# Performance work log

Measured on AMD Instinct MI355X. Metric: run time of the kernel, lower is better.

Reference implementation:

```python
import jax, jax.numpy as jnp
import numpy as np

B, L, D = 16, 256, 256        # batch, enc positions, enc_out_dim
H, E, V, T = 256, 256, 172, 128  # dec_rnn_h, emb_size, vocab, target_len
INIT = 0.01


def setup_inputs() -> dict:
    key = jax.random.key(0)
    ks = jax.random.split(key, 20)
    u = lambda k, shape, s: jax.random.uniform(k, shape, jnp.float32, -s, s)
    inp = {
        "imgs": jax.random.normal(ks[0], (B, L, D), jnp.float32),
        "target_list": jax.random.randint(ks[1], (B, T), 0, V),
        # embedding + LSTMCell (torch layout: W_ih [4H, H+E], W_hh [4H, H])
        "emb": jax.random.normal(ks[2], (V, E), jnp.float32) * 0.02,
        "W_ih": u(ks[3], (4 * H, H + E), 1.0 / np.sqrt(H)),
        "W_hh": u(ks[4], (4 * H, H), 1.0 / np.sqrt(H)),
        "b_ih": u(ks[5], (4 * H,), 1.0 / np.sqrt(H)),
        "b_hh": u(ks[6], (4 * H,), 1.0 / np.sqrt(H)),
        # attention / output projections (no bias)
        "W1": u(ks[7], (D, D), 1.0 / np.sqrt(D)),
        "W2": u(ks[8], (D, H), 1.0 / np.sqrt(H)),
        "W3": u(ks[9], (H, H + D), 1.0 / np.sqrt(H + D)),
        "Wout": u(ks[10], (V, H), 1.0 / np.sqrt(H)),
        "beta": u(ks[11], (D,), INIT),
        # init decoder linears (with bias)
        "wh_W": u(ks[12], (H, D), 1.0 / np.sqrt(D)),
        "wh_b": u(ks[13], (H,), 1.0 / np.sqrt(D)),
        "wc_W": u(ks[14], (H, D), 1.0 / np.sqrt(D)),
        "wc_b": u(ks[15], (H,), 1.0 / np.sqrt(D)),
        "wo_W": u(ks[16], (H, D), 1.0 / np.sqrt(D)),
        "wo_b": u(ks[17], (H,), 1.0 / np.sqrt(D)),
    }
    return inp


def _forward(imgs, emb, W_ih, W_hh, b_ih, b_hh, W1, W2, W3, Wout, beta,
             wh_W, wh_b, wc_W, wc_b, wo_W, wo_b, target_list):
    # init states from mean-pooled encoder output
    mean_enc = imgs.mean(axis=1)                       # [B, D]
    h = jnp.tanh(mean_enc @ wh_W.T + wh_b)             # [B, H]
    c = jnp.tanh(mean_enc @ wc_W.T + wc_b)
    o = jnp.tanh(mean_enc @ wo_W.T + wo_b)

    enc_proj = jnp.einsum('bld,ed->ble', imgs, W1)     # W_1(enc_out), step-invariant

    def step(carry, tgt_t):
        h, c, o = carry
        prev_y = emb[tgt_t]                            # [B, E]
        inp = jnp.concatenate([prev_y, o], axis=1)     # [B, E+H]
        gates = inp @ W_ih.T + b_ih + h @ W_hh.T + b_hh  # [B, 4H]
        i_g, f_g, g_g, o_g = jnp.split(gates, 4, axis=1)
        c_new = jax.nn.sigmoid(f_g) * c + jax.nn.sigmoid(i_g) * jnp.tanh(g_g)
        h_new = jax.nn.sigmoid(o_g) * jnp.tanh(c_new)
        # Bahdanau attention
        alpha = jnp.tanh(enc_proj + (h_new @ W2.T)[:, None, :])   # [B, L, D]
        score = jnp.einsum('bld,d->bl', alpha, beta)
        attn = jax.nn.softmax(score, axis=-1)                     # [B, L]
        ctx = jnp.einsum('bl,bld->bd', attn, imgs)                # [B, D]
        o_new = jnp.tanh(jnp.concatenate([h_new, ctx], axis=1) @ W3.T)  # [B, H]
        logit = jax.nn.softmax(o_new @ Wout.T, axis=1)            # [B, V]
        return (h_new, c_new, o_new), logit

    _, logits = jax.lax.scan(step, (h, c, o), target_list.T)      # [T, B, V]
    return jnp.transpose(logits, (1, 0, 2))                       # [B, T, V]


def reference(imgs, target_list, emb, W_ih, W_hh, b_ih, b_hh, W1, W2, W3,
              Wout, beta, wh_W, wh_b, wc_W, wc_b, wo_W, wo_b):
    return _forward(imgs, emb, W_ih, W_hh, b_ih, b_hh, W1, W2, W3, Wout, beta,
                    wh_W, wh_b, wc_W, wc_b, wo_W, wo_b, target_list)
```

## Files before the change

### kernel.cpp

```cpp
#include <hip/hip_runtime.h>

typedef unsigned int u32;


#define OFF_BAR   0ull
#define OFF_PSE   16384ull
#define OFF_STH   65536ull
#define OFF_PQH   98304ull
#define OFF_PCTX  622592ull
#define OFF_OALL  1146880ull
#define OFF_GTOK  3244032ull

__device__ __forceinline__ float sigm(float x){ return 1.0f/(1.0f+__expf(-x)); }
__device__ __forceinline__ float tanh_f(float x){ return 1.0f - 2.0f/(1.0f+__expf(2.0f*x)); }

__device__ __forceinline__ float blo(u32 q){ u32 x = q<<16; float f; __builtin_memcpy(&f,&x,4); return f; }
__device__ __forceinline__ float bhi(u32 q){ u32 x = q & 0xffff0000u; float f; __builtin_memcpy(&f,&x,4); return f; }
__device__ __forceinline__ u32 f2bu(float f){ u32 x; __builtin_memcpy(&x,&f,4); x = x + 0x7fffu + ((x>>16)&1u); return x>>16; }

struct F8 { float v[8]; };
__device__ __forceinline__ F8 ld8f(const float* q){
  F8 r; float4 a = *(const float4*)q; float4 b = *(const float4*)(q+4);
  r.v[0]=a.x;r.v[1]=a.y;r.v[2]=a.z;r.v[3]=a.w;r.v[4]=b.x;r.v[5]=b.y;r.v[6]=b.z;r.v[7]=b.w;
  return r;
}
__device__ __forceinline__ float dot8(const F8& w, const float* x){
  float4 a = *(const float4*)x; float4 b = *(const float4*)(x+4);
  return w.v[0]*a.x + w.v[1]*a.y + w.v[2]*a.z + w.v[3]*a.w
       + w.v[4]*b.x + w.v[5]*b.y + w.v[6]*b.z + w.v[7]*b.w;
}
__device__ __forceinline__ float dot8r(const float* wr, const float* x){
  float4 a = *(const float4*)x; float4 b = *(const float4*)(x+4);
  return wr[0]*a.x + wr[1]*a.y + wr[2]*a.z + wr[3]*a.w
       + wr[4]*b.x + wr[5]*b.y + wr[6]*b.z + wr[7]*b.w;
}

__device__ __forceinline__ float cohload(const float* p){
  u32 x = __hip_atomic_load((const u32*)p, __ATOMIC_RELAXED, __HIP_MEMORY_SCOPE_AGENT);
  float f; __builtin_memcpy(&f,&x,4); return f;
}
__device__ __forceinline__ void cohstore(float* p, float v){
  u32 x; __builtin_memcpy(&x,&v,4);
  __hip_atomic_store((u32*)p, x, __ATOMIC_RELAXED, __HIP_MEMORY_SCOPE_AGENT);
}

__device__ __forceinline__ void wait_flags(u32* gf, u32 seq){
  if (threadIdx.x < 16){
    while (__hip_atomic_load(gf + threadIdx.x*16, __ATOMIC_RELAXED, __HIP_MEMORY_SCOPE_AGENT) < seq){
      __builtin_amdgcn_s_sleep(1);
    }
  }
  __syncthreads();
}
__device__ __forceinline__ void publish_flag(u32* myf, u32 seq){
  __hip_atomic_store(myf, seq, __ATOMIC_RELEASE, __HIP_MEMORY_SCOPE_AGENT);
}
__device__ __forceinline__ void publish_flag_fast(u32* myf, u32 seq){
  asm volatile("s_waitcnt vmcnt(0)" ::: "memory");
  __hip_atomic_store(myf, seq, __ATOMIC_RELAXED, __HIP_MEMORY_SCOPE_AGENT);
}

extern "C" __global__ __launch_bounds__(256)
void k_init(char* __restrict__ ws){
  u32* bar = (u32*)(ws + OFF_BAR);
  const int gt = blockIdx.x*256 + threadIdx.x;
  if (gt < 4096) bar[gt] = 0u;
}

extern "C" __global__ __launch_bounds__(256, 1)
void k_main(const float* __restrict__ imgs, const int* __restrict__ tgt,
            const float* __restrict__ emb,  const float* __restrict__ W_ih,
            const float* __restrict__ W_hh, const float* __restrict__ b_ih,
            const float* __restrict__ b_hh, const float* __restrict__ W1,
            const float* __restrict__ W2,   const float* __restrict__ W3,
            const float* __restrict__ beta, const float* __restrict__ whW,
            const float* __restrict__ whb,  const float* __restrict__ wcW,
            const float* __restrict__ wcb,  const float* __restrict__ woW,
            const float* __restrict__ wob,  char* __restrict__ ws)
{
  const int tid = threadIdx.x, bid = blockIdx.x;
  const int g = bid & 15, w = bid >> 4, u0 = w*16;

  u32* gf   = (u32*)(ws + OFF_BAR) + g*256;
  u32* myf  = gf + w*16;
  float* stH  = (float*)(ws + OFF_STH);
  float* pQH  = (float*)(ws + OFF_PQH);
  float* pCTX = (float*)(ws + OFF_PCTX);
  float* pSE  = (float*)(ws + OFF_PSE);
  float* oAll = (float*)(ws + OFF_OALL);
  float* gtok = (float*)(ws + OFF_GTOK);

  __shared__ __align__(16) float sImg[16*256];
  __shared__ __align__(16) float sEnc[16*256];
  __shared__ __align__(16) float sPimg[16*256];
  __shared__ __align__(16) float sPool[768];
  __shared__ __align__(16) float sHprev[256];
  __shared__ __align__(16) float sO[256];
  __shared__ __align__(16) float sHw2[256];
  __shared__ float sBeta[256];
  __shared__ float sG[64];
  __shared__ float sHown[16];
  __shared__ float sC[16];
  __shared__ float sE[16];
  __shared__ float sE2[16];

  sBeta[tid] = beta[tid];

  for (int r=0; r<3; r++){
    const int tk = bid + 256*r;
    __syncthreads();
    if (tk < 688){
      const int v = tk>>2, q = tk&3;
      sPool[512 + tid] = emb[(size_t)v*256 + tid];
      __syncthreads();
      const int j = q*256 + tid;
      const float* wr = W_ih + (size_t)j*512;
      float a = 0.f;
      #pragma unroll 8
      for (int c=0; c<32; c++) a += dot8(ld8f(wr + c*8), sPool + 512 + c*8);
      gtok[(size_t)v*1024 + j] = a + b_ih[j] + b_hh[j];
    } else {
      __syncthreads();
    }
  }
  __syncthreads();

  { const size_t r0 = (size_t)(g*256 + w*16);
    for (int ri=0; ri<16; ri++) sImg[ri*256+tid] = imgs[(r0+ri)*256 + tid];
    __syncthreads();
    { float acc[16];
      #pragma unroll
      for (int ri=0; ri<16; ri++) acc[ri]=0.f;
      const float* w1r = W1 + (size_t)tid*256;
      for (int c=0; c<32; c++){
        F8 wv = ld8f(w1r + c*8);
        #pragma unroll
        for (int ri=0; ri<16; ri++) acc[ri] += dot8(wv, sImg + ri*256 + c*8);
      }
      for (int ri=0; ri<16; ri++) sEnc[ri*256+tid] = acc[ri];
    }
    { float acc[16];
      #pragma unroll
      for (int ri=0; ri<16; ri++) acc[ri]=0.f;
      const float* w3cr = W3 + (size_t)tid*512 + 256;
      for (int c=0; c<32; c++){
        F8 wv = ld8f(w3cr + c*8);
        #pragma unroll
        for (int ri=0; ri<16; ri++) acc[ri] += dot8(wv, sImg + ri*256 + c*8);
      }
      for (int ri=0; ri<16; ri++) sPimg[ri*256+tid] = acc[ri];
    }
  }
  __syncthreads();

  { float m = 0.f;
    for (int l=0; l<256; l++) m += imgs[((size_t)g*256 + l)*256 + tid];
    sPool[tid] = m * (1.0f/256.0f);
  }
  __syncthreads();
  { const float* whr = whW + (size_t)tid*256;
    const float* wor = woW + (size_t)tid*256;
    float ah=0.f, ao=0.f;
    for (int c=0; c<32; c++){
      ah += dot8(ld8f(whr + c*8), sPool + c*8);
      ao += dot8(ld8f(wor + c*8), sPool + c*8);
    }
    sHprev[tid] = tanhf(ah + whb[tid]);
    sO[tid]     = tanhf(ao + wob[tid]);
  }
  { const int j = tid>>4, sub = tid&15, u = u0 + j;
    float ac=0.f;
    #pragma unroll
    for (int c=0; c<2; c++)
      ac += dot8(ld8f(wcW + (size_t)u*256 + sub*16 + c*8), sPool + sub*16 + c*8);
    ac += __shfl_xor(ac,1); ac += __shfl_xor(ac,2); ac += __shfl_xor(ac,4); ac += __shfl_xor(ac,8);
    if (sub == 0) sC[j] = tanhf(ac + wcb[u]);
  }

  const int rl = tid>>2, p = tid&3;
  const int unit = rl & 15, gate = rl >> 4;
  const int grow = gate*256 + u0 + unit;
  float wior[64], whhr[64];
  { const float* wio = W_ih + (size_t)grow*512 + 256 + p*64;
    const float* whh = W_hh + (size_t)grow*256 +       p*64;
    #pragma unroll
    for (int c=0; c<8; c++){
      F8 a = ld8f(wio + c*8);
      F8 b = ld8f(whh + c*8);
      #pragma unroll
      for (int i=0; i<8; i++){ wior[c*8+i] = a.v[i]; whhr[c*8+i] = b.v[i]; }
    }
  }
  u32 w2p[128];
  { const float* w2r = W2 + (size_t)tid*256;
    #pragma unroll
    for (int c=0; c<128; c++)
      w2p[c] = f2bu(w2r[2*c]) | (f2bu(w2r[2*c+1]) << 16);
  }
  float w3h[16];
  { F8 a = ld8f(W3 + (size_t)tid*512 + u0);
    F8 b = ld8f(W3 + (size_t)tid*512 + u0 + 8);
    #pragma unroll
    for (int i=0; i<8; i++){ w3h[i] = a.v[i]; w3h[8+i] = b.v[i]; }
  }
  const int* tgt_g = tgt + g*128;
  const float* gtok_row = gtok + grow;

  __syncthreads();
  if (tid == 0) publish_flag(myf, 1u);
  wait_flags(gf, 1u);

  float hpart = 0.f;
  { const float* xh = sHprev + p*64;
    #pragma unroll
    for (int c=0; c<8; c++) hpart += dot8r(whhr + c*8, xh + c*8);
  }

  for (int t=0; t<128; t++){
    const int par = t & 1;
    const int y = tgt_g[t];
    const float gyv = gtok_row[(size_t)y*1024];

    { float acc = hpart;
      const float* xo = sO + p*64;
      #pragma unroll
      for (int c=0; c<8; c++) acc += dot8r(wior + c*8, xo + c*8);
      acc += __shfl_xor(acc, 1); acc += __shfl_xor(acc, 2);
      if (p == 0) sG[rl] = acc + gyv;
    }
    __syncthreads();
    if (tid < 16){
      float ig = sG[tid], fg = sG[16+tid], gg = sG[32+tid], og = sG[48+tid];
      float cn = sigm(fg)*sC[tid] + sigm(ig)*tanh_f(gg);
      float hn = sigm(og)*tanh_f(cn);
      sC[tid] = cn;
      sHown[tid] = hn;
      cohstore(stH + par*4096 + g*256 + u0 + tid, hn);
      if (tid == 0) publish_flag_fast(myf, 2u*t + 2u);
    }
    __syncthreads();
    { float qh = 0.f;
      #pragma unroll
      for (int k=0; k<16; k++) qh += w3h[k] * sHown[k];
      cohstore(pQH + ((size_t)(par*16 + g)*16 + w)*256 + tid, qh);
    }

    wait_flags(gf, 2u*t + 2u);
    sHprev[tid] = cohload(stH + par*4096 + g*256 + tid);
    __syncthreads();
    { float a = 0.f;
      #pragma unroll
      for (int c=0; c<128; c++){
        u32 q = w2p[c];
        a += blo(q)*sHprev[2*c] + bhi(q)*sHprev[2*c+1];
      }
      sHw2[tid] = a;
    }
    __syncthreads();
    { const int li = tid>>4, sub = tid&15;
      const float* ep = sEnc + li*256;
      float sc = 0.f;
      #pragma unroll
      for (int i=0; i<16; i++){ int d = i*16 + sub; sc += tanh_f(ep[d] + sHw2[d]) * sBeta[d]; }
      sc += __shfl_xor(sc,1); sc += __shfl_xor(sc,2); sc += __shfl_xor(sc,4); sc += __shfl_xor(sc,8);
      if (sub == 0) sE[li] = __expf(sc);
    }
    __syncthreads();
    { float pv = 0.f;
      #pragma unroll
      for (int li2=0; li2<16; li2++) pv += sE[li2] * sPimg[li2*256 + tid];
      cohstore(pCTX + ((size_t)g*16 + w)*256 + tid, pv);
    }
    if (tid == 0){
      float se = 0.f;
      #pragma unroll
      for (int j=0; j<16; j++) se += sE[j];
      cohstore(pSE + g*16 + w, se);
    }
    __syncthreads();
    if (tid == 0) publish_flag_fast(myf, 2u*t + 3u);

    wait_flags(gf, 2u*t + 3u);
    if (tid < 16) sE2[tid] = cohload(pSE + g*16 + tid);
    float qh = 0.f, pvs = 0.f;
    { const float* qb = pQH  + (size_t)(par*16 + g)*4096 + tid;
      const float* cb = pCTX + (size_t)g*4096 + tid;
      #pragma unroll
      for (int j=0; j<16; j++){ qh += cohload(qb + j*256); pvs += cohload(cb + j*256); }
    }
    __syncthreads();
    { float se = 0.f;
      #pragma unroll
      for (int j=0; j<16; j++) se += sE2[j];
      float o = tanh_f(qh + pvs/se);
      sO[tid] = o;
      if ((tid>>4) == w) oAll[((size_t)t*16 + g)*256 + tid] = o;
    }
    { float hp2 = 0.f;
      const float* xh = sHprev + p*64;
      #pragma unroll
      for (int c=0; c<8; c++) hp2 += dot8r(whhr + c*8, xh + c*8);
      hpart = hp2;
    }
    __syncthreads();
  }
}

extern "C" __global__ __launch_bounds__(256)
void k_logits(const float* __restrict__ Wout, char* __restrict__ ws, float* __restrict__ out){
  __shared__ __align__(16) float sO_[256];
  __shared__ __align__(16) float sRed[256];
  const int tid = threadIdx.x, q = blockIdx.x;
  const int b = q >> 7, t = q & 127;
  const float* oAll = (const float*)(ws + OFF_OALL);
  sO_[tid] = oAll[((size_t)t*16 + b)*256 + tid];
  __syncthreads();
  float lg = 0.f;
  if (tid < 172){
    const float* wr = Wout + (size_t)tid*256;
    #pragma unroll 8
    for (int c=0; c<32; c++) lg += dot8(ld8f(wr + c*8), sO_ + c*8);
  }
  sRed[tid] = (tid < 172) ? lg : -1e30f;
  __syncthreads();
  for (int s2=128; s2>0; s2>>=1){ if (tid < s2) sRed[tid] = fmaxf(sRed[tid], sRed[tid+s2]); __syncthreads(); }
  const float mx = sRed[0];
  __syncthreads();
  const float ev = (tid < 172) ? __expf(lg - mx) : 0.f;
  sRed[tid] = ev;
  __syncthreads();
  for (int s2=128; s2>0; s2>>=1){ if (tid < s2) sRed[tid] += sRed[tid+s2]; __syncthreads(); }
  const float inv = 1.0f / sRed[0];
  if (tid < 172) out[((size_t)b*128 + t)*172 + tid] = ev * inv;
}

extern "C" void kernel_launch(void* const* d_in, const int* in_sizes, int n_in,
                              void* d_out, int out_size, void* d_ws, size_t ws_size,
                              hipStream_t stream) {
  (void)in_sizes; (void)n_in; (void)out_size; (void)ws_size;
  char* ws = (char*)d_ws;
  k_init<<<16, 256, 0, stream>>>(ws);
  k_main<<<256, 256, 0, stream>>>(
      (const float*)d_in[0],  (const int*)d_in[1],  (const float*)d_in[2],
      (const float*)d_in[3],  (const float*)d_in[4], (const float*)d_in[5],
      (const float*)d_in[6],  (const float*)d_in[7], (const float*)d_in[8],
      (const float*)d_in[9],  (const float*)d_in[11], (const float*)d_in[12],
      (const float*)d_in[13], (const float*)d_in[14], (const float*)d_in[15],
      (const float*)d_in[16], (const float*)d_in[17], ws);
  k_logits<<<2048, 256, 0, stream>>>((const float*)d_in[10], ws, (float*)d_out);
}
```

Baseline: 1.462 ms.

## Repartition recurrent kernel into 8 wider blocks per batch with 512 threads

Changes the persistent recurrent kernel from 256 blocks of 256 threads (16 blocks per batch row, 16 hidden units each) to 128 blocks of 512 threads (8 blocks per batch row, 32 units each). Cross-block flag waits and partial-sum reductions (qh, ctx, softmax denominators) shrink from 16 to 8 contributors, which cuts inter-block synchronisation and coherent global traffic per timestep. Thread pairs now split dot products and combine them with shuffles, and the W_hh partial for the next step is moved ahead of the second publish. The cost is larger shared memory per block and more register pressure at 512 threads, which could lower occupancy or force spills.

```diff
diff --git a/kernel.cpp b/kernel.cpp
--- a/kernel.cpp
+++ b/kernel.cpp
@@ -5,11 +5,11 @@
 
 #define OFF_BAR   0ull
 #define OFF_PSE   16384ull
-#define OFF_STH   65536ull
-#define OFF_PQH   98304ull
-#define OFF_PCTX  622592ull
-#define OFF_OALL  1146880ull
-#define OFF_GTOK  3244032ull
+#define OFF_STH   32768ull
+#define OFF_PQH   65536ull
+#define OFF_PCTX  327680ull
+#define OFF_OALL  458752ull
+#define OFF_GTOK  2555904ull
 
 __device__ __forceinline__ float sigm(float x){ return 1.0f/(1.0f+__expf(-x)); }
 __device__ __forceinline__ float tanh_f(float x){ return 1.0f - 2.0f/(1.0f+__expf(2.0f*x)); }
@@ -45,7 +45,7 @@
 }
 
 __device__ __forceinline__ void wait_flags(u32* gf, u32 seq){
-  if (threadIdx.x < 16){
+  if (threadIdx.x < 8){
     while (__hip_atomic_load(gf + threadIdx.x*16, __ATOMIC_RELAXED, __HIP_MEMORY_SCOPE_AGENT) < seq){
       __builtin_amdgcn_s_sleep(1);
     }
@@ -64,10 +64,10 @@
 void k_init(char* __restrict__ ws){
   u32* bar = (u32*)(ws + OFF_BAR);
   const int gt = blockIdx.x*256 + threadIdx.x;
-  if (gt < 4096) bar[gt] = 0u;
-}
-
-extern "C" __global__ __launch_bounds__(256, 1)
+  if (gt < 2048) bar[gt] = 0u;
+}
+
+extern "C" __global__ __launch_bounds__(512, 2)
 void k_main(const float* __restrict__ imgs, const int* __restrict__ tgt,
             const float* __restrict__ emb,  const float* __restrict__ W_ih,
             const float* __restrict__ W_hh, const float* __restrict__ b_ih,
@@ -79,9 +79,9 @@
             const float* __restrict__ wob,  char* __restrict__ ws)
 {
   const int tid = threadIdx.x, bid = blockIdx.x;
-  const int g = bid & 15, w = bid >> 4, u0 = w*16;
-
-  u32* gf   = (u32*)(ws + OFF_BAR) + g*256;
+  const int g = bid & 15, w = bid >> 4, u0 = w*32;
+
+  u32* gf   = (u32*)(ws + OFF_BAR) + g*128;
   u32* myf  = gf + w*16;
   float* stH  = (float*)(ws + OFF_STH);
   float* pQH  = (float*)(ws + OFF_PQH);
@@ -90,34 +90,34 @@
   float* oAll = (float*)(ws + OFF_OALL);
   float* gtok = (float*)(ws + OFF_GTOK);
 
-  __shared__ __align__(16) float sImg[16*256];
-  __shared__ __align__(16) float sEnc[16*256];
-  __shared__ __align__(16) float sPimg[16*256];
-  __shared__ __align__(16) float sPool[768];
+  __shared__ __align__(16) float sImg[32*256];
+  __shared__ __align__(16) float sEnc[32*256];
+  __shared__ __align__(16) float sPimg[32*256];
+  __shared__ __align__(16) float sPool[256];
   __shared__ __align__(16) float sHprev[256];
   __shared__ __align__(16) float sO[256];
   __shared__ __align__(16) float sHw2[256];
   __shared__ float sBeta[256];
-  __shared__ float sG[64];
-  __shared__ float sHown[16];
-  __shared__ float sC[16];
-  __shared__ float sE[16];
-  __shared__ float sE2[16];
-
-  sBeta[tid] = beta[tid];
+  __shared__ float sG[128];
+  __shared__ float sHown[32];
+  __shared__ float sC[32];
+  __shared__ float sE[32];
+  __shared__ float sE2[8];
+
+  if (tid < 256) sBeta[tid] = beta[tid];
 
   for (int r=0; r<3; r++){
-    const int tk = bid + 256*r;
-    __syncthreads();
-    if (tk < 688){
-      const int v = tk>>2, q = tk&3;
-      sPool[512 + tid] = emb[(size_t)v*256 + tid];
+    const int tk = bid + 128*r;
+    __syncthreads();
+    if (tk < 344){
+      const int v = tk>>1, h2 = tk&1;
+      if (tid < 256) sPool[tid] = emb[(size_t)v*256 + tid];
       __syncthreads();
-      const int j = q*256 + tid;
+      const int j = h2*512 + tid;
       const float* wr = W_ih + (size_t)j*512;
       float a = 0.f;
       #pragma unroll 8
-      for (int c=0; c<32; c++) a += dot8(ld8f(wr + c*8), sPool + 512 + c*8);
+      for (int c=0; c<32; c++) a += dot8(ld8f(wr + c*8), sPool + c*8);
       gtok[(size_t)v*1024 + j] = a + b_ih[j] + b_hh[j];
     } else {
       __syncthreads();
@@ -125,61 +125,70 @@
   }
   __syncthreads();
 
-  { const size_t r0 = (size_t)(g*256 + w*16);
-    for (int ri=0; ri<16; ri++) sImg[ri*256+tid] = imgs[(r0+ri)*256 + tid];
+  { const size_t r0 = (size_t)(g*256 + w*32);
+    const int dcol = tid & 255, rh = tid >> 8;
+    for (int ri=0; ri<16; ri++)
+      sImg[(rh*16+ri)*256 + dcol] = imgs[(r0 + rh*16 + ri)*256 + dcol];
     __syncthreads();
     { float acc[16];
       #pragma unroll
       for (int ri=0; ri<16; ri++) acc[ri]=0.f;
-      const float* w1r = W1 + (size_t)tid*256;
+      const float* w1r = W1 + (size_t)dcol*256;
       for (int c=0; c<32; c++){
         F8 wv = ld8f(w1r + c*8);
         #pragma unroll
-        for (int ri=0; ri<16; ri++) acc[ri] += dot8(wv, sImg + ri*256 + c*8);
-      }
-      for (int ri=0; ri<16; ri++) sEnc[ri*256+tid] = acc[ri];
+        for (int ri=0; ri<16; ri++) acc[ri] += dot8(wv, sImg + (rh*16+ri)*256 + c*8);
+      }
+      for (int ri=0; ri<16; ri++) sEnc[(rh*16+ri)*256 + dcol] = acc[ri];
     }
     { float acc[16];
       #pragma unroll
       for (int ri=0; ri<16; ri++) acc[ri]=0.f;
-      const float* w3cr = W3 + (size_t)tid*512 + 256;
+      const float* w3cr = W3 + (size_t)dcol*512 + 256;
       for (int c=0; c<32; c++){
         F8 wv = ld8f(w3cr + c*8);
         #pragma unroll
-        for (int ri=0; ri<16; ri++) acc[ri] += dot8(wv, sImg + ri*256 + c*8);
-      }
-      for (int ri=0; ri<16; ri++) sPimg[ri*256+tid] = acc[ri];
-    }
-  }
-  __syncthreads();
-
-  { float m = 0.f;
-    for (int l=0; l<256; l++) m += imgs[((size_t)g*256 + l)*256 + tid];
-    sPool[tid] = m * (1.0f/256.0f);
-  }
-  __syncthreads();
-  { const float* whr = whW + (size_t)tid*256;
-    const float* wor = woW + (size_t)tid*256;
+        for (int ri=0; ri<16; ri++) acc[ri] += dot8(wv, sImg + (rh*16+ri)*256 + c*8);
+      }
+      for (int ri=0; ri<16; ri++) sPimg[(rh*16+ri)*256 + dcol] = acc[ri];
+    }
+  }
+  __syncthreads();
+
+  { const int d = tid>>1, lh = tid&1;
+    float m = 0.f;
+    for (int l=lh*128; l<lh*128+128; l++) m += imgs[((size_t)g*256 + l)*256 + d];
+    m += __shfl_xor(m, 1);
+    if (lh == 0) sPool[d] = m * (1.0f/256.0f);
+  }
+  __syncthreads();
+  { const int u = tid>>1, ch = tid&1;
+    const float* whr = whW + (size_t)u*256 + ch*128;
+    const float* wor = woW + (size_t)u*256 + ch*128;
     float ah=0.f, ao=0.f;
-    for (int c=0; c<32; c++){
-      ah += dot8(ld8f(whr + c*8), sPool + c*8);
-      ao += dot8(ld8f(wor + c*8), sPool + c*8);
-    }
-    sHprev[tid] = tanhf(ah + whb[tid]);
-    sO[tid]     = tanhf(ao + wob[tid]);
-  }
-  { const int j = tid>>4, sub = tid&15, u = u0 + j;
+    for (int c=0; c<16; c++){
+      ah += dot8(ld8f(whr + c*8), sPool + ch*128 + c*8);
+      ao += dot8(ld8f(wor + c*8), sPool + ch*128 + c*8);
+    }
+    ah += __shfl_xor(ah,1); ao += __shfl_xor(ao,1);
+    if (ch == 0){
+      sHprev[u] = tanhf(ah + whb[u]);
+      sO[u]     = tanhf(ao + wob[u]);
+    }
+  }
+  { const int ul = tid>>4, sub = tid&15;
+    const int u = u0 + ul;
     float ac=0.f;
     #pragma unroll
     for (int c=0; c<2; c++)
       ac += dot8(ld8f(wcW + (size_t)u*256 + sub*16 + c*8), sPool + sub*16 + c*8);
     ac += __shfl_xor(ac,1); ac += __shfl_xor(ac,2); ac += __shfl_xor(ac,4); ac += __shfl_xor(ac,8);
-    if (sub == 0) sC[j] = tanhf(ac + wcb[u]);
+    if (sub == 0) sC[ul] = tanhf(ac + wcb[u]);
   }
 
   const int rl = tid>>2, p = tid&3;
-  const int unit = rl & 15, gate = rl >> 4;
-  const int grow = gate*256 + u0 + unit;
+  const int ul_g = rl & 31, gate = rl >> 5;
+  const int grow = gate*256 + u0 + ul_g;
   float wior[64], whhr[64];
   { const float* wio = W_ih + (size_t)grow*512 + 256 + p*64;
     const float* whh = W_hh + (size_t)grow*256 +       p*64;
@@ -191,15 +200,17 @@
       for (int i=0; i<8; i++){ wior[c*8+i] = a.v[i]; whhr[c*8+i] = b.v[i]; }
     }
   }
-  u32 w2p[128];
-  { const float* w2r = W2 + (size_t)tid*256;
-    #pragma unroll
-    for (int c=0; c<128; c++)
+  const int d2 = tid>>1, ch2 = tid&1;
+  u32 w2p[64];
+  { const float* w2r = W2 + (size_t)d2*256 + ch2*128;
+    #pragma unroll
+    for (int c=0; c<64; c++)
       w2p[c] = f2bu(w2r[2*c]) | (f2bu(w2r[2*c+1]) << 16);
   }
+  const int uq = tid>>1, kh = tid&1;
   float w3h[16];
-  { F8 a = ld8f(W3 + (size_t)tid*512 + u0);
-    F8 b = ld8f(W3 + (size_t)tid*512 + u0 + 8);
+  { F8 a = ld8f(W3 + (size_t)uq*512 + u0 + kh*16);
+    F8 b = ld8f(W3 + (size_t)uq*512 + u0 + kh*16 + 8);
     #pragma unroll
     for (int i=0; i<8; i++){ w3h[i] = a.v[i]; w3h[8+i] = b.v[i]; }
   }
@@ -229,8 +240,8 @@
       if (p == 0) sG[rl] = acc + gyv;
     }
     __syncthreads();
-    if (tid < 16){
-      float ig = sG[tid], fg = sG[16+tid], gg = sG[32+tid], og = sG[48+tid];
+    if (tid < 32){
+      float ig = sG[tid], fg = sG[32+tid], gg = sG[64+tid], og = sG[96+tid];
       float cn = sigm(fg)*sC[tid] + sigm(ig)*tanh_f(gg);
       float hn = sigm(og)*tanh_f(cn);
       sC[tid] = cn;
@@ -241,20 +252,23 @@
     __syncthreads();
     { float qh = 0.f;
       #pragma unroll
-      for (int k=0; k<16; k++) qh += w3h[k] * sHown[k];
-      cohstore(pQH + ((size_t)(par*16 + g)*16 + w)*256 + tid, qh);
+      for (int i=0; i<16; i++) qh += w3h[i] * sHown[kh*16 + i];
+      qh += __shfl_xor(qh, 1);
+      if (kh == 0) cohstore(pQH + ((size_t)(par*16 + g)*8 + w)*256 + uq, qh);
     }
 
     wait_flags(gf, 2u*t + 2u);
-    sHprev[tid] = cohload(stH + par*4096 + g*256 + tid);
+    if (tid < 256) sHprev[tid] = cohload(stH + par*4096 + g*256 + tid);
     __syncthreads();
     { float a = 0.f;
-      #pragma unroll
-      for (int c=0; c<128; c++){
+      const float* hb = sHprev + ch2*128;
+      #pragma unroll
+      for (int c=0; c<64; c++){
         u32 q = w2p[c];
-        a += blo(q)*sHprev[2*c] + bhi(q)*sHprev[2*c+1];
-      }
-      sHw2[tid] = a;
+        a += blo(q)*hb[2*c] + bhi(q)*hb[2*c+1];
+      }
+      a += __shfl_xor(a, 1);
+      if (ch2 == 0) sHw2[d2] = a;
     }
     __syncthreads();
     { const int li = tid>>4, sub = tid&15;
@@ -267,40 +281,49 @@
     }
     __syncthreads();
     { float pv = 0.f;
-      #pragma unroll
-      for (int li2=0; li2<16; li2++) pv += sE[li2] * sPimg[li2*256 + tid];
-      cohstore(pCTX + ((size_t)g*16 + w)*256 + tid, pv);
+      const int lh = kh;
+      #pragma unroll
+      for (int li2=0; li2<16; li2++) pv += sE[lh*16 + li2] * sPimg[(lh*16 + li2)*256 + uq];
+      pv += __shfl_xor(pv, 1);
+      if (kh == 0) cohstore(pCTX + ((size_t)g*8 + w)*256 + uq, pv);
     }
     if (tid == 0){
       float se = 0.f;
       #pragma unroll
-      for (int j=0; j<16; j++) se += sE[j];
-      cohstore(pSE + g*16 + w, se);
-    }
-    __syncthreads();
-    if (tid == 0) publish_flag_fast(myf, 2u*t + 3u);
-
-    wait_flags(gf, 2u*t + 3u);
-    if (tid < 16) sE2[tid] = cohload(pSE + g*16 + tid);
-    float qh = 0.f, pvs = 0.f;
-    { const float* qb = pQH  + (size_t)(par*16 + g)*4096 + tid;
-      const float* cb = pCTX + (size_t)g*4096 + tid;
-      #pragma unroll
-      for (int j=0; j<16; j++){ qh += cohload(qb + j*256); pvs += cohload(cb + j*256); }
-    }
-    __syncthreads();
-    { float se = 0.f;
-      #pragma unroll
-      for (int j=0; j<16; j++) se += sE2[j];
-      float o = tanh_f(qh + pvs/se);
-      sO[tid] = o;
-      if ((tid>>4) == w) oAll[((size_t)t*16 + g)*256 + tid] = o;
+      for (int j=0; j<32; j++) se += sE[j];
+      cohstore(pSE + g*8 + w, se);
     }
     { float hp2 = 0.f;
       const float* xh = sHprev + p*64;
       #pragma unroll
       for (int c=0; c<8; c++) hp2 += dot8r(whhr + c*8, xh + c*8);
       hpart = hp2;
+    }
+    __syncthreads();
+    if (tid == 0) publish_flag_fast(myf, 2u*t + 3u);
+
+    wait_flags(gf, 2u*t + 3u);
+    if (tid < 8) sE2[tid] = cohload(pSE + g*8 + tid);
+    float qh = 0.f, pvs = 0.f;
+    { const float* qb = pQH  + (size_t)(par*16 + g)*2048 + uq;
+      const float* cb = pCTX + (size_t)g*2048 + uq;
+      #pragma unroll
+      for (int j=0; j<4; j++){
+        qh  += cohload(qb + (kh*4 + j)*256);
+        pvs += cohload(cb + (kh*4 + j)*256);
+      }
+      qh  += __shfl_xor(qh, 1);
+      pvs += __shfl_xor(pvs, 1);
+    }
+    __syncthreads();
+    { float se = 0.f;
+      #pragma unroll
+      for (int j=0; j<8; j++) se += sE2[j];
+      float o = tanh_f(qh + pvs/se);
+      if (kh == 0){
+        sO[uq] = o;
+        if ((uq>>5) == w) oAll[((size_t)t*16 + g)*256 + uq] = o;
+      }
     }
     __syncthreads();
   }
@@ -339,8 +362,8 @@
                               hipStream_t stream) {
   (void)in_sizes; (void)n_in; (void)out_size; (void)ws_size;
   char* ws = (char*)d_ws;
-  k_init<<<16, 256, 0, stream>>>(ws);
-  k_main<<<256, 256, 0, stream>>>(
+  k_init<<<8, 256, 0, stream>>>(ws);
+  k_main<<<128, 512, 0, stream>>>(
       (const float*)d_in[0],  (const int*)d_in[1],  (const float*)d_in[2],
       (const float*)d_in[3],  (const float*)d_in[4], (const float*)d_in[5],
       (const float*)d_in[6],  (const float*)d_in[7], (const float*)d_in[8],
```

Result: slower. 4.529 ms (+209.8%).
